# Optimization experiments

Measured on AMD Instinct MI355X. Metric: run time of the kernel, lower is better.

Reference implementation:

```python
import jax, jax.numpy as jnp
import numpy as np

LAMBDA_TEMP = 20.0
GAMMA = 20.0
MARGIN = 0.05
EPS = 1e-8

B, K, M, D = 128, 256, 8, 128


def _unit(x, axis=-1):
    return x / jnp.linalg.norm(x, axis=axis, keepdims=True)


def setup_inputs() -> dict:
    key = jax.random.key(0)
    k1, k2, k3 = jax.random.split(key, 3)
    v_proj = _unit(jax.random.normal(k1, (B, K, D), dtype=jnp.float32))
    prototypes = _unit(jax.random.normal(k2, (K, M, D), dtype=jnp.float32))
    concept_labels = jax.random.randint(k3, (B, K), 0, 2, dtype=jnp.int64)
    return {"v_proj": v_proj, "concept_labels": concept_labels, "prototypes": prototypes}


def reference(v_proj, concept_labels, prototypes):
    # all-pairs prototype similarities: query vector (b,k) vs prototypes of concept c
    # sims: (B, K, C, M)
    sims = jnp.einsum('bkd,cmd->bkcm', v_proj, prototypes)
    # Eq.6: soft assignment over the M prototypes of each concept
    q = jax.nn.softmax(GAMMA * sims, axis=-1)
    # Eq.7-8: weighted similarity sim_c(v)  -> (B, K, C)
    sim = jnp.sum(q * sims, axis=-1)
    # positive similarity: concept k queried against its own prototypes, plus margin
    sim_pos = jnp.einsum('bkk->bk', sim) + MARGIN  # (B, K)
    # Eq.9: -log( exp(lam*sim_pos) / (sum_c exp(lam*sim_c) + eps) )
    denom = jnp.sum(jnp.exp(LAMBDA_TEMP * sim), axis=-1) + EPS  # (B, K)
    loss_bk = jnp.log(denom) - LAMBDA_TEMP * sim_pos  # (B, K)
    mask = (concept_labels == 1).astype(loss_bk.dtype)
    num_pos = jnp.sum(mask)
    total = jnp.sum(loss_bk * mask)
    return jnp.where(num_pos > 0, total / num_pos, total)
```

## Files before the change

kernel.cpp:

```cpp
#include <hip/hip_runtime.h>

#define LT     20.0f
#define C2EXP  28.853900817779268f
#define CHUNKS 16
#define NBLK   512

typedef _Float16 half8 __attribute__((ext_vector_type(8)));
typedef float    f32x4 __attribute__((ext_vector_type(4)));

#if __has_builtin(__builtin_amdgcn_exp2f)
#define EXP2F(x) __builtin_amdgcn_exp2f(x)
#else
#define EXP2F(x) __expf(0.69314718055994531f * (x))
#endif

__device__ __forceinline__ float swz16(float x) {
    return __int_as_float(__builtin_amdgcn_ds_swizzle(__float_as_int(x), 0x401F));
}

__global__ __launch_bounds__(256)
void mpcl_prep(const float* __restrict__ P, _Float16* __restrict__ Pw,
               int* __restrict__ ws)
{
    int id = blockIdx.x * 256 + threadIdx.x;
    if (id == 0) ws[0] = 0;
    int ch    = id >> 11;
    int colq  = (id >> 9) & 3;
    int cfrag = (id >> 6) & 7;
    int lane  = id & 63;
    int n = lane & 15, q = lane >> 4;
    int c = cfrag & 3, h = cfrag >> 2;
    int col  = colq * 32 + ((n >> 2) << 3) + (n & 3) + (h << 2);
    int gcol = (ch << 7) + col;
    const float* src = P + ((size_t)gcol << 7) + c * 32 + q * 8;
    float4 a = *(const float4*)src;
    float4 b = *(const float4*)(src + 4);
    half8 hv;
    hv[0] = (_Float16)a.x; hv[1] = (_Float16)a.y;
    hv[2] = (_Float16)a.z; hv[3] = (_Float16)a.w;
    hv[4] = (_Float16)b.x; hv[5] = (_Float16)b.y;
    hv[6] = (_Float16)b.z; hv[7] = (_Float16)b.w;
    *(half8*)(Pw + (size_t)id * 8) = hv;
}

__global__ __launch_bounds__(512, 4)
void mpcl_main(const float* __restrict__ V,
               const int*   __restrict__ labels,
               const _Float16* __restrict__ Pw,
               int* __restrict__ ws,
               float* __restrict__ out)
{
    __shared__ float sh_denom[64];
    __shared__ float sh_simpos[64];
    __shared__ float sh_fin[16];
    __shared__ int   sh_last;

    int*   gcnt = ws;
    float* part = (float*)((char*)ws + 256);

    const int tid  = threadIdx.x;
    const int lane = tid & 63;
    const int w    = tid >> 6;
    const int colq = w & 3;
    const int rg   = w >> 2;
    const int n    = lane & 15;
    const int q    = lane >> 4;
    const int rowbase = blockIdx.x * 64;

    if (tid < 64) { sh_denom[tid] = 0.0f; sh_simpos[tid] = 0.0f; }

    int lab = 0;
    if (tid < 64) lab = labels[rowbase + tid];

    half8 vh[2][4];
#pragma unroll
    for (int rf = 0; rf < 2; ++rf) {
        const float* vr = V + ((size_t)(rowbase + rg * 32 + rf * 16 + n) << 7) + q * 8;
#pragma unroll
        for (int c = 0; c < 4; ++c) {
            float4 x0 = *(const float4*)(vr + c * 32);
            float4 x1 = *(const float4*)(vr + c * 32 + 4);
            vh[rf][c][0] = (_Float16)x0.x; vh[rf][c][1] = (_Float16)x0.y;
            vh[rf][c][2] = (_Float16)x0.z; vh[rf][c][3] = (_Float16)x0.w;
            vh[rf][c][4] = (_Float16)x1.x; vh[rf][c][5] = (_Float16)x1.y;
            vh[rf][c][6] = (_Float16)x1.z; vh[rf][c][7] = (_Float16)x1.w;
        }
    }
    __syncthreads();

    const half8* pw = (const half8*)Pw + (size_t)colq * 512 + lane;

    const int rowk0 = (rowbase + rg * 32 + n) & 255;
    const int rowk1 = (rowbase + rg * 32 + 16 + n) & 255;

    float dn0 = 0.f, dn1 = 0.f;

    half8 bufA[8], bufB[8];
#pragma unroll
    for (int f = 0; f < 8; ++f) bufA[f] = pw[f * 64];

#define COMPUTE(BUF, CABASE) do {                                               \
    f32x4 acc1[2] = {{0.f,0.f,0.f,0.f},{0.f,0.f,0.f,0.f}};                      \
    f32x4 acc2[2] = {{0.f,0.f,0.f,0.f},{0.f,0.f,0.f,0.f}};                      \
    _Pragma("unroll")                                                           \
    for (int c = 0; c < 4; ++c) {                                               \
        acc1[0] = __builtin_amdgcn_mfma_f32_16x16x32_f16(BUF[c],   vh[0][c], acc1[0], 0, 0, 0); \
        acc1[1] = __builtin_amdgcn_mfma_f32_16x16x32_f16(BUF[c],   vh[1][c], acc1[1], 0, 0, 0); \
        acc2[0] = __builtin_amdgcn_mfma_f32_16x16x32_f16(BUF[4+c], vh[0][c], acc2[0], 0, 0, 0); \
        acc2[1] = __builtin_amdgcn_mfma_f32_16x16x32_f16(BUF[4+c], vh[1][c], acc2[1], 0, 0, 0); \
    }                                                                           \
    _Pragma("unroll")                                                           \
    for (int rf = 0; rf < 2; ++rf) {                                            \
        float x0 = acc1[rf][0], x1 = acc1[rf][1], x2 = acc1[rf][2], x3 = acc1[rf][3]; \
        float x4 = acc2[rf][0], x5 = acc2[rf][1], x6 = acc2[rf][2], x7 = acc2[rf][3]; \
        float e0 = EXP2F(C2EXP * x0), e1 = EXP2F(C2EXP * x1);                   \
        float e2 = EXP2F(C2EXP * x2), e3 = EXP2F(C2EXP * x3);                   \
        float e4 = EXP2F(C2EXP * x4), e5 = EXP2F(C2EXP * x5);                   \
        float e6 = EXP2F(C2EXP * x6), e7 = EXP2F(C2EXP * x7);                   \
        float es = ((e0 + e1) + (e2 + e3)) + ((e4 + e5) + (e6 + e7));           \
        float ss = fmaf(e0, x0, fmaf(e1, x1, fmaf(e2, x2, e3 * x3)))            \
                 + fmaf(e4, x4, fmaf(e5, x5, fmaf(e6, x6, e7 * x7)));           \
        float simc = __fdividef(ss, es);                                        \
        if (rf) dn1 += EXP2F(C2EXP * simc); else dn0 += EXP2F(C2EXP * simc);    \
        if ((CABASE) == (rf ? rowk1 : rowk0))                                   \
            sh_simpos[rg * 32 + rf * 16 + n] = simc;         \
    }                                                                           \
} while (0)

    int cA = colq * 4 + q;
#pragma unroll 1
    for (int ch = 0; ch < CHUNKS; ch += 2) {
#pragma unroll
        for (int f = 0; f < 8; ++f) bufB[f] = pw[(ch + 1) * 2048 + f * 64];

        COMPUTE(bufA, cA);

        if (ch + 2 < CHUNKS) {
#pragma unroll
            for (int f = 0; f < 8; ++f) bufA[f] = pw[(ch + 2) * 2048 + f * 64];
        }

        COMPUTE(bufB, cA + 16);
        cA += 32;
    }

#pragma unroll
    for (int rf = 0; rf < 2; ++rf) {
        float t = rf ? dn1 : dn0;
        t += swz16(t);
        t += __shfl_xor(t, 32);
        if (lane < 16)
            atomicAdd(&sh_denom[rg * 32 + rf * 16 + n], t);
    }
    __syncthreads();

    float s = 0.f, cc = 0.f;
    if (tid < 64) {
        float lp = logf(sh_denom[tid] + 1e-8f) - LT * (sh_simpos[tid] + 0.05f);
        float mk = (lab == 1) ? 1.0f : 0.0f;
        s = lp * mk;
        cc = mk;
    }
#pragma unroll
    for (int off = 32; off >= 1; off >>= 1) {
        s  += __shfl_down(s, off);
        cc += __shfl_down(cc, off);
    }

    if (tid == 0) {
        __hip_atomic_store(&part[2 * blockIdx.x],     s,  __ATOMIC_RELAXED, __HIP_MEMORY_SCOPE_AGENT);
        __hip_atomic_store(&part[2 * blockIdx.x + 1], cc, __ATOMIC_RELAXED, __HIP_MEMORY_SCOPE_AGENT);
        __threadfence();
        int g = __hip_atomic_fetch_add(gcnt, 1, __ATOMIC_ACQ_REL, __HIP_MEMORY_SCOPE_AGENT);
        sh_last = (g == NBLK - 1);
    }
    __syncthreads();
    if (sh_last) {
        float ts = 0.f, tc = 0.f;
        for (int i = tid; i < NBLK; i += 512) {
            ts += __hip_atomic_load(&part[2 * i],     __ATOMIC_RELAXED, __HIP_MEMORY_SCOPE_AGENT);
            tc += __hip_atomic_load(&part[2 * i + 1], __ATOMIC_RELAXED, __HIP_MEMORY_SCOPE_AGENT);
        }
#pragma unroll
        for (int off = 32; off >= 1; off >>= 1) {
            ts += __shfl_down(ts, off);
            tc += __shfl_down(tc, off);
        }
        if (lane == 0) { sh_fin[w] = ts; sh_fin[8 + w] = tc; }
        __syncthreads();
        if (tid == 0) {
            ts = 0.f; tc = 0.f;
#pragma unroll
            for (int i = 0; i < 8; ++i) { ts += sh_fin[i]; tc += sh_fin[8 + i]; }
            out[0] = (tc > 0.0f) ? (ts / tc) : ts;
        }
    }
}

extern "C" void kernel_launch(void* const* d_in, const int* in_sizes, int n_in,
                              void* d_out, int out_size, void* d_ws, size_t ws_size,
                              hipStream_t stream)
{
    const float* V      = (const float*)d_in[0];
    const int*   labels = (const int*)d_in[1];
    const float* P      = (const float*)d_in[2];
    float* out = (float*)d_out;
    int*   ws  = (int*)d_ws;
    _Float16* Pw = (_Float16*)((char*)d_ws + 16384);

    mpcl_prep<<<128, 256, 0, stream>>>(P, Pw, ws);
    mpcl_main<<<NBLK, 512, 0, stream>>>(V, labels, Pw, ws, out);
}
```

Baseline: 111.7 us.

## Stage prototype chunks into LDS double buffer via direct global-to-LDS loads

Each block now copies each prototype chunk once into a shared-memory double buffer using the direct global-to-LDS load builtin. The MFMA operands are then read from LDS, replacing the per-wave register prefetch from global memory. Waves in different row groups no longer fetch the same prototype data twice, and register pressure drops. In exchange, each chunk needs a block-wide barrier, and the kernel uses 64KB of shared memory per block, which may limit how many blocks fit on a CU.

```diff
diff --git a/kernel.cpp b/kernel.cpp
--- a/kernel.cpp
+++ b/kernel.cpp
@@ -17,6 +17,10 @@
 __device__ __forceinline__ float swz16(float x) {
     return __int_as_float(__builtin_amdgcn_ds_swizzle(__float_as_int(x), 0x401F));
 }
+
+#define GLD16(gp, lp) __builtin_amdgcn_global_load_lds( \
+    (const __attribute__((address_space(1))) void*)(gp), \
+    (__attribute__((address_space(3))) void*)(lp), 16, 0, 0)
 
 __global__ __launch_bounds__(256)
 void mpcl_prep(const float* __restrict__ P, _Float16* __restrict__ Pw,
@@ -43,13 +47,15 @@
     *(half8*)(Pw + (size_t)id * 8) = hv;
 }
 
-__global__ __launch_bounds__(512, 4)
+__global__ __attribute__((amdgpu_flat_work_group_size(512, 512),
+                          amdgpu_waves_per_eu(4, 4)))
 void mpcl_main(const float* __restrict__ V,
                const int*   __restrict__ labels,
                const _Float16* __restrict__ Pw,
                int* __restrict__ ws,
                float* __restrict__ out)
 {
+    __shared__ __align__(16) _Float16 Pst[2][2048 * 8];
     __shared__ float sh_denom[64];
     __shared__ float sh_simpos[64];
     __shared__ float sh_fin[16];
@@ -72,6 +78,19 @@
     int lab = 0;
     if (tid < 64) lab = labels[rowbase + tid];
 
+    const _Float16* gbase = Pw + (size_t)(w * 256 + lane) * 8;
+
+#define STAGE(CH, B) do {                                       \
+    const _Float16* g_ = gbase + (size_t)(CH) * 16384;          \
+    _Float16* l_ = &Pst[B][(w * 256) * 8];                      \
+    GLD16(g_,        l_);                                       \
+    GLD16(g_ +  512, l_ +  512);                                \
+    GLD16(g_ + 1024, l_ + 1024);                                \
+    GLD16(g_ + 1536, l_ + 1536);                                \
+} while (0)
+
+    STAGE(0, 0);
+
     half8 vh[2][4];
 #pragma unroll
     for (int rf = 0; rf < 2; ++rf) {
@@ -86,62 +105,51 @@
             vh[rf][c][6] = (_Float16)x1.z; vh[rf][c][7] = (_Float16)x1.w;
         }
     }
-    __syncthreads();
-
-    const half8* pw = (const half8*)Pw + (size_t)colq * 512 + lane;
 
     const int rowk0 = (rowbase + rg * 32 + n) & 255;
     const int rowk1 = (rowbase + rg * 32 + 16 + n) & 255;
+    const int aoff  = (colq * 512 + lane) * 8;
 
     float dn0 = 0.f, dn1 = 0.f;
-
-    half8 bufA[8], bufB[8];
-#pragma unroll
-    for (int f = 0; f < 8; ++f) bufA[f] = pw[f * 64];
-
-#define COMPUTE(BUF, CABASE) do {                                               \
-    f32x4 acc1[2] = {{0.f,0.f,0.f,0.f},{0.f,0.f,0.f,0.f}};                      \
-    f32x4 acc2[2] = {{0.f,0.f,0.f,0.f},{0.f,0.f,0.f,0.f}};                      \
-    _Pragma("unroll")                                                           \
-    for (int c = 0; c < 4; ++c) {                                               \
-        acc1[0] = __builtin_amdgcn_mfma_f32_16x16x32_f16(BUF[c],   vh[0][c], acc1[0], 0, 0, 0); \
-        acc1[1] = __builtin_amdgcn_mfma_f32_16x16x32_f16(BUF[c],   vh[1][c], acc1[1], 0, 0, 0); \
-        acc2[0] = __builtin_amdgcn_mfma_f32_16x16x32_f16(BUF[4+c], vh[0][c], acc2[0], 0, 0, 0); \
-        acc2[1] = __builtin_amdgcn_mfma_f32_16x16x32_f16(BUF[4+c], vh[1][c], acc2[1], 0, 0, 0); \
-    }                                                                           \
-    _Pragma("unroll")                                                           \
-    for (int rf = 0; rf < 2; ++rf) {                                            \
-        float x0 = acc1[rf][0], x1 = acc1[rf][1], x2 = acc1[rf][2], x3 = acc1[rf][3]; \
-        float x4 = acc2[rf][0], x5 = acc2[rf][1], x6 = acc2[rf][2], x7 = acc2[rf][3]; \
-        float e0 = EXP2F(C2EXP * x0), e1 = EXP2F(C2EXP * x1);                   \
-        float e2 = EXP2F(C2EXP * x2), e3 = EXP2F(C2EXP * x3);                   \
-        float e4 = EXP2F(C2EXP * x4), e5 = EXP2F(C2EXP * x5);                   \
-        float e6 = EXP2F(C2EXP * x6), e7 = EXP2F(C2EXP * x7);                   \
-        float es = ((e0 + e1) + (e2 + e3)) + ((e4 + e5) + (e6 + e7));           \
-        float ss = fmaf(e0, x0, fmaf(e1, x1, fmaf(e2, x2, e3 * x3)))            \
-                 + fmaf(e4, x4, fmaf(e5, x5, fmaf(e6, x6, e7 * x7)));           \
-        float simc = __fdividef(ss, es);                                        \
-        if (rf) dn1 += EXP2F(C2EXP * simc); else dn0 += EXP2F(C2EXP * simc);    \
-        if ((CABASE) == (rf ? rowk1 : rowk0))                                   \
-            sh_simpos[rg * 32 + rf * 16 + n] = simc;         \
-    }                                                                           \
-} while (0)
-
     int cA = colq * 4 + q;
+
 #pragma unroll 1
-    for (int ch = 0; ch < CHUNKS; ch += 2) {
-#pragma unroll
-        for (int f = 0; f < 8; ++f) bufB[f] = pw[(ch + 1) * 2048 + f * 64];
-
-        COMPUTE(bufA, cA);
-
-        if (ch + 2 < CHUNKS) {
-#pragma unroll
-            for (int f = 0; f < 8; ++f) bufA[f] = pw[(ch + 2) * 2048 + f * 64];
-        }
-
-        COMPUTE(bufB, cA + 16);
-        cA += 32;
+    for (int ch = 0; ch < CHUNKS; ++ch) {
+        __syncthreads();
+
+        if (ch + 1 < CHUNKS) STAGE(ch + 1, (ch + 1) & 1);
+
+        const _Float16* base = &Pst[ch & 1][0];
+
+        f32x4 acc1[2] = {{0.f,0.f,0.f,0.f},{0.f,0.f,0.f,0.f}};
+        f32x4 acc2[2] = {{0.f,0.f,0.f,0.f},{0.f,0.f,0.f,0.f}};
+#pragma unroll
+        for (int c = 0; c < 4; ++c) {
+            half8 a1 = *(const half8*)&base[aoff + c * 512];
+            half8 a2 = *(const half8*)&base[aoff + c * 512 + 2048];
+            acc1[0] = __builtin_amdgcn_mfma_f32_16x16x32_f16(a1, vh[0][c], acc1[0], 0, 0, 0);
+            acc1[1] = __builtin_amdgcn_mfma_f32_16x16x32_f16(a1, vh[1][c], acc1[1], 0, 0, 0);
+            acc2[0] = __builtin_amdgcn_mfma_f32_16x16x32_f16(a2, vh[0][c], acc2[0], 0, 0, 0);
+            acc2[1] = __builtin_amdgcn_mfma_f32_16x16x32_f16(a2, vh[1][c], acc2[1], 0, 0, 0);
+        }
+
+#pragma unroll
+        for (int rf = 0; rf < 2; ++rf) {
+            float x0 = acc1[rf][0], x1 = acc1[rf][1], x2 = acc1[rf][2], x3 = acc1[rf][3];
+            float x4 = acc2[rf][0], x5 = acc2[rf][1], x6 = acc2[rf][2], x7 = acc2[rf][3];
+            float e0 = EXP2F(C2EXP * x0), e1 = EXP2F(C2EXP * x1);
+            float e2 = EXP2F(C2EXP * x2), e3 = EXP2F(C2EXP * x3);
+            float e4 = EXP2F(C2EXP * x4), e5 = EXP2F(C2EXP * x5);
+            float e6 = EXP2F(C2EXP * x6), e7 = EXP2F(C2EXP * x7);
+            float es = ((e0 + e1) + (e2 + e3)) + ((e4 + e5) + (e6 + e7));
+            float ss = fmaf(e0, x0, fmaf(e1, x1, fmaf(e2, x2, e3 * x3)))
+                     + fmaf(e4, x4, fmaf(e5, x5, fmaf(e6, x6, e7 * x7)));
+            float simc = __fdividef(ss, es);
+            if (rf) dn1 += EXP2F(C2EXP * simc); else dn0 += EXP2F(C2EXP * simc);
+            if (cA == (rf ? rowk1 : rowk0))
+                sh_simpos[rg * 32 + rf * 16 + n] = simc;
+        }
+        cA += 16;
     }
 
 #pragma unroll
```

Result: faster. 108.9 us (-2.5%).
